# Kernel optimization log

Hardware: AMD Instinct MI355X
Metric: run time of the kernel (lower is better)

Reference implementation:

```python
import jax, jax.numpy as jnp
import numpy as np

K = 3      # kernel size
PAD = 1    # padding


def _conv(x, w, b=None):
    y = jax.lax.conv_general_dilated(
        x, w, window_strides=(1, 1), padding=((PAD, PAD), (PAD, PAD)),
        dimension_numbers=('NCHW', 'OIHW', 'NCHW'))
    if b is not None:
        y = y + b[None, :, None, None]
    return y


def _deform_conv2d(x, offset, mask, weight):
    # torchvision deform_conv2d with offset_groups == C (one offset pair per
    # input channel per kernel tap), stride=1, dilation=1, zero padding.
    B, C, H, W = x.shape
    KK = K * K
    off = offset.reshape(B, C, KK, 2, H, W)   # [...,0]=dy, [...,1]=dx
    dy, dx = off[:, :, :, 0], off[:, :, :, 1]
    m = mask.reshape(B, C, KK, H, W)

    ki = (jnp.arange(KK) // K).reshape(1, 1, KK, 1, 1).astype(x.dtype)
    kj = (jnp.arange(KK) % K).reshape(1, 1, KK, 1, 1).astype(x.dtype)
    gy = jnp.arange(H, dtype=x.dtype).reshape(1, 1, 1, H, 1)
    gx = jnp.arange(W, dtype=x.dtype).reshape(1, 1, 1, 1, W)
    py = dy + gy - PAD + ki   # sampling y coords, [B,C,KK,H,W]
    px = dx + gx - PAD + kj   # sampling x coords

    # torchvision: sample is zero unless -1 < p < size
    valid = (py > -1) & (py < H) & (px > -1) & (px < W)
    y0f = jnp.floor(py)
    x0f = jnp.floor(px)
    wy = py - y0f
    wx = px - x0f
    y0 = y0f.astype(jnp.int32)
    x0 = x0f.astype(jnp.int32)
    y1 = y0 + 1
    x1 = x0 + 1

    xf = x.reshape(B, C, H * W)

    def gather(yi, xi):
        inb = (yi >= 0) & (yi < H) & (xi >= 0) & (xi < W)
        yc = jnp.clip(yi, 0, H - 1)
        xc = jnp.clip(xi, 0, W - 1)
        idx = (yc * W + xc).reshape(B, C, -1)
        v = jnp.take_along_axis(xf, idx, axis=2).reshape(yi.shape)
        return jnp.where(inb, v, jnp.zeros((), x.dtype))

    val = ((1 - wy) * (1 - wx) * gather(y0, x0)
           + (1 - wy) * wx * gather(y0, x1)
           + wy * (1 - wx) * gather(y1, x0)
           + wy * wx * gather(y1, x1))
    samp = jnp.where(valid, val, jnp.zeros((), x.dtype)) * m   # [B,C,KK,H,W]

    O = weight.shape[0]
    return jnp.einsum('bckhw,ock->bohw', samp, weight.reshape(O, C, KK))


def setup_inputs() -> dict:
    key = jax.random.key(0)
    k1, k2, k3, k4, k5, k6 = jax.random.split(key, 6)
    B, C, O, H, W = 8, 64, 128, 64, 64
    KK = K * K
    x = jax.random.normal(k1, (B, C, H, W), dtype=jnp.float32)
    # offset conv: 2*C*KK output channels (module inits to 0; use small random
    # weights so the irregular sampling path is exercised)
    w_off = jax.random.normal(k2, (2 * C * KK, C, K, K), dtype=jnp.float32) * 0.05
    b_off = jnp.zeros((2 * C * KK,), dtype=jnp.float32)
    w_mod = jax.random.normal(k3, (C * KK, C, K, K), dtype=jnp.float32) * 0.05
    b_mod = jax.random.normal(k4, (C * KK,), dtype=jnp.float32) * 0.05
    w_conv = jax.random.normal(k5, (O, C, K, K), dtype=jnp.float32) / np.sqrt(C * KK)
    return {"x": x, "w_off": w_off, "b_off": b_off,
            "w_mod": w_mod, "b_mod": b_mod, "w_conv": w_conv}


def reference(x, w_off, b_off, w_mod, b_mod, w_conv):
    H, W = x.shape[2], x.shape[3]
    max_off = max(H, W) / 4.0
    offset = jnp.clip(_conv(x, w_off, b_off), -max_off, max_off)
    mask = _conv(x, w_mod, b_mod)
    return _deform_conv2d(x, offset, mask, w_conv)
```

## Files before the change

### kernel.cpp

```cpp
#include <hip/hip_runtime.h>
#include <cstddef>
#include <cstdint>

#define TCNT 256

namespace {
constexpr int CIN    = 64;
constexpr int COUT   = 128;
constexpr int HDIM   = 64;
constexpr int WDIM   = 64;
constexpr int HW     = HDIM * WDIM;
constexpr int KD     = CIN * 9;
constexpr int NOFF   = 2 * CIN * 9;
constexpr int NTOT   = NOFF + CIN * 9;
constexpr int NBATCH = 8;
constexpr int HXW    = 66;
constexpr int COPAD  = 1792;
constexpr int NGT    = COPAD / 16;
constexpr float MAXOFF = 16.0f;

constexpr size_t XT_ELEMS = (size_t)NBATCH * HXW * HXW * 64;
constexpr size_t WP_ELEMS = (size_t)18 * NGT * 512;
constexpr size_t WC_ELEMS = (size_t)18 * 8 * 512;
constexpr size_t OFF_XFH  = 0;
constexpr size_t OFF_WPH  = XT_ELEMS;
constexpr size_t OFF_WPL  = XT_ELEMS + WP_ELEMS;
constexpr size_t OFF_WCH  = XT_ELEMS + 2 * WP_ELEMS;
constexpr size_t FIXED_BYTES = (XT_ELEMS + 2 * WP_ELEMS + WC_ELEMS) * 2;
}

typedef __attribute__((ext_vector_type(8))) short    s16x8;
typedef __attribute__((ext_vector_type(8))) _Float16 f16x8;
typedef __attribute__((ext_vector_type(4))) float    f32x4;

__device__ __forceinline__ unsigned short f2h(float v) {
  _Float16 h = (_Float16)v;
  return __builtin_bit_cast(unsigned short, h);
}
__device__ __forceinline__ float h2f(unsigned short u) {
  return (float)__builtin_bit_cast(_Float16, u);
}

__global__ __launch_bounds__(TCNT) void prep_x(
    const float* __restrict__ x, unsigned short* __restrict__ xFh)
{
  const int b  = blockIdx.y;
  const int yy = blockIdx.x;
  const int t  = threadIdx.x;
  unsigned short* oh = xFh + ((size_t)(b * HXW + yy)) * HXW * 64;
  if (yy == 0 || yy == HXW - 1) {
    for (int lin = t; lin < HXW * 64; lin += TCNT) oh[lin] = 0;
    return;
  }
  __shared__ float tile[64][65];
  const int y = yy - 1;
  #pragma unroll
  for (int i = 0; i < 4; ++i) {
    const int f = t + TCNT * i;
    const int c = f >> 4, xq = f & 15;
    const float4 v =
        *(const float4*)(x + ((size_t)(b * 64 + c)) * HW + y * WDIM + xq * 4);
    tile[c][xq * 4 + 0] = v.x; tile[c][xq * 4 + 1] = v.y;
    tile[c][xq * 4 + 2] = v.z; tile[c][xq * 4 + 3] = v.w;
  }
  if (t < 128) {
    const int c = t & 63, xe = (t >> 6) ? (HXW - 1) * 64 : 0;
    oh[xe + c] = 0;
  }
  __syncthreads();
  const int xc = t >> 2, cg = (t & 3) * 16;
  s16x8 h0, h1;
  #pragma unroll
  for (int u = 0; u < 8; ++u) h0[u] = (short)f2h(tile[cg + u][xc]);
  #pragma unroll
  for (int u = 0; u < 8; ++u) h1[u] = (short)f2h(tile[cg + 8 + u][xc]);
  *(s16x8*)(oh + (xc + 1) * 64 + cg)     = h0;
  *(s16x8*)(oh + (xc + 1) * 64 + cg + 8) = h1;
}

__global__ __launch_bounds__(TCNT) void prep_w(
    const float* __restrict__ w_off, const float* __restrict__ w_mod,
    unsigned short* __restrict__ wF1h, unsigned short* __restrict__ wF1l)
{
  const int g  = blockIdx.x;
  const int hh = blockIdx.y;
  const int r  = hh >> 1, ks = hh & 1;
  const int t  = threadIdx.x;
  const size_t base = ((size_t)hh * NGT + g) * 512;
  #pragma unroll
  for (int q = 0; q < 2; ++q) {
    const int e = t + q * 256;
    const int l = e >> 3, f = e & 7;
    const int co = g * 16 + (l & 15);
    const int c  = ks * 32 + (l >> 4) * 8 + f;
    float v = 0.f;
    if (co < NOFF)      v = w_off[(size_t)co * KD + c * 9 + r];
    else if (co < NTOT) v = w_mod[(size_t)(co - NOFF) * KD + c * 9 + r];
    const unsigned short hb = f2h(v);
    wF1h[base + e] = hb;
    wF1l[base + e] = f2h(v - h2f(hb));
  }
}

__global__ __launch_bounds__(TCNT) void prep_wc(
    const float* __restrict__ w_conv, unsigned short* __restrict__ wF2)
{
  const int nt = blockIdx.x;
  const int hh = blockIdx.y;
  const int sc = hh >> 1, ks = hh & 1;
  const int t  = threadIdx.x;
  const size_t base = ((size_t)hh * 8 + nt) * 512;
  #pragma unroll
  for (int q = 0; q < 2; ++q) {
    const int e = t + q * 256;
    const int l = e >> 3, f = e & 7;
    const int o = nt * 16 + (l & 15);
    const int c = sc * 64 + ks * 32 + (l >> 4) * 8 + f;
    wF2[base + e] = f2h(w_conv[(size_t)o * KD + c]);
  }
}

__global__ __launch_bounds__(TCNT, 3) void dcn_stage1(
    const unsigned short* __restrict__ xFh,
    const unsigned short* __restrict__ wF1h, const unsigned short* __restrict__ wF1l,
    const float* __restrict__ b_off, const float* __restrict__ b_mod,
    float* __restrict__ ws, int b0, int nb)
{
  __shared__ unsigned short Ah[2][128][32];

  const int t      = threadIdx.x;
  const int Mchunk = nb * HW;
  const int p0  = blockIdx.x * 128;
  const int b   = b0 + (p0 >> 12);
  const int h0  = (p0 & (HW - 1)) >> 6;
  const int co0 = blockIdx.y * 128;

  const int s_row = t >> 1;
  const int s_kh  = t & 1;
  const int s_sw  = ((s_row >> 1) & 3) << 3;
  const int a_h   = h0 + (s_row >> 6);
  const int a_w   = s_row & 63;
  const unsigned short* xbh = xFh + (size_t)b * HXW * HXW * 64;

  const int wave = t >> 6, lane = t & 63;
  const int wm = wave >> 1, wn = wave & 1;
  const int lrow = lane & 15;
  const int lkh  = lane >> 4;
  const int gbase = (co0 >> 4) + wn * 4;

  f32x4 acc[4][4];
  #pragma unroll
  for (int m = 0; m < 4; ++m)
    #pragma unroll
    for (int n = 0; n < 4; ++n) acc[m][n] = (f32x4)0.f;

  s16x8 rE0, rE1, rO0, rO1;
  f16x8 wh[4], wl[4];

#define ALOAD(D0, D1, H)                                                     \
  {                                                                          \
    const int r_  = (H) >> 1;                                                \
    const int ks_ = (H) & 1;                                                 \
    const int ki_ = r_ / 3;                                                  \
    const int kj_ = r_ - 3 * ki_;                                            \
    const size_t aoff_ = ((size_t)((a_h + ki_) * HXW + (a_w + kj_))) * 64 +  \
                         ks_ * 32 + s_kh * 16;                               \
    D0 = *(const s16x8*)(xbh + aoff_);                                       \
    D1 = *(const s16x8*)(xbh + aoff_ + 8);                                   \
  }

#define AWRITE(S0, S1, SEL)                                                  \
  {                                                                          \
    const int c0_ = (s_kh * 16) ^ s_sw;                                      \
    const int c1_ = (s_kh * 16 + 8) ^ s_sw;                                  \
    *(s16x8*)&Ah[SEL][s_row][c0_] = S0;                                      \
    *(s16x8*)&Ah[SEL][s_row][c1_] = S1;                                      \
  }

#define WLOAD(H)                                                             \
  {                                                                          \
    _Pragma("unroll")                                                        \
    for (int n = 0; n < 4; ++n) {                                            \
      const size_t o_ = ((size_t)(H) * NGT + gbase + n) * 512 + lane * 8;    \
      wh[n] = *(const f16x8*)(wF1h + o_);                                    \
      wl[n] = *(const f16x8*)(wF1l + o_);                                    \
    }                                                                        \
  }

#define MFMA_P(SEL)                                                          \
  {                                                                          \
    f16x8 fa[4];                                                             \
    _Pragma("unroll")                                                        \
    for (int m = 0; m < 4; ++m) {                                            \
      const int row = wm * 64 + m * 16 + lrow;                               \
      const int col = (lkh * 8) ^ (((row >> 1) & 3) << 3);                   \
      fa[m] = *(const f16x8*)&Ah[SEL][row][col];                             \
    }                                                                        \
    _Pragma("unroll")                                                        \
    for (int n = 0; n < 4; ++n) {                                            \
      _Pragma("unroll")                                                      \
      for (int m = 0; m < 4; ++m) {                                          \
        acc[m][n] = __builtin_amdgcn_mfma_f32_16x16x32_f16(fa[m], wh[n], acc[m][n], 0, 0, 0); \
        acc[m][n] = __builtin_amdgcn_mfma_f32_16x16x32_f16(fa[m], wl[n], acc[m][n], 0, 0, 0); \
      }                                                                      \
    }                                                                        \
  }

  ALOAD(rE0, rE1, 0)
  WLOAD(0)
  AWRITE(rE0, rE1, 0)
  ALOAD(rO0, rO1, 1)
  __syncthreads();

  #pragma unroll 1
  for (int h = 0; h < 17; ++h) {
    MFMA_P(h & 1)
    WLOAD(h + 1)
    if ((h & 1) == 0) {
      AWRITE(rO0, rO1, 1)
      if (h < 16) ALOAD(rE0, rE1, h + 2)
    } else {
      AWRITE(rE0, rE1, 0)
      if (h < 16) ALOAD(rO0, rO1, h + 2)
    }
    __syncthreads();
  }
  MFMA_P(1)

  const bool isOff = (co0 < NOFF);
  #pragma unroll
  for (int n = 0; n < 4; ++n) {
    const int cog = co0 + wn * 64 + n * 16 + lrow;
    if (cog >= NTOT) continue;
    const float bias = isOff ? b_off[cog] : b_mod[cog - NOFF];
    float* oplane = ws + (size_t)cog * Mchunk;
    #pragma unroll
    for (int m = 0; m < 4; ++m) {
      f32x4 v = acc[m][n];
      float4 o;
      o.x = v[0] + bias; o.y = v[1] + bias; o.z = v[2] + bias; o.w = v[3] + bias;
      if (isOff) {
        o.x = fminf(MAXOFF, fmaxf(-MAXOFF, o.x));
        o.y = fminf(MAXOFF, fmaxf(-MAXOFF, o.y));
        o.z = fminf(MAXOFF, fmaxf(-MAXOFF, o.z));
        o.w = fminf(MAXOFF, fmaxf(-MAXOFF, o.w));
      }
      const int pb = p0 + wm * 64 + m * 16 + lkh * 4;
      *(float4*)(oplane + pb) = o;
    }
  }
#undef ALOAD
#undef AWRITE
#undef WLOAD
#undef MFMA_P
}

__global__ __launch_bounds__(TCNT) void dcn_stage2(
    const float* __restrict__ x, const float* __restrict__ planes,
    const unsigned short* __restrict__ wF2,
    float* __restrict__ out, int b0, int nb)
{
  __shared__ unsigned short SH[2][32][64], SL[2][32][64];

  const int t      = threadIdx.x;
  const int Mchunk = nb * HW;
  const int pc0 = blockIdx.x * 32;
  const int b   = b0 + (pc0 >> 12);
  const int h   = (pc0 & (HW - 1)) >> 6;
  const int w0  = pc0 & 63;

  const int tpx = t & 31;
  const int tsg = t >> 5;
  const int a_swz = (tpx & 7) << 3;
  const float* ws_pix = planes + pc0 + tpx;
  const float* xb     = x + (size_t)b * CIN * HW;

  const int wave = t >> 6, lane = t & 63;
  const int lrow = lane & 15, lkh = lane >> 4;
  const int f_swz = (lrow & 7) << 3;

  f32x4 acc[2][2];
  #pragma unroll
  for (int m = 0; m < 2; ++m)
    #pragma unroll
    for (int n = 0; n < 2; ++n) acc[m][n] = (f32x4)0.f;

  float vals[8];
  f16x8 w4A[4], w4B[4];

#define SAMPLE(SCC)                                                          \
  {                                                                          \
    _Pragma("unroll")                                                        \
    for (int j = 0; j < 8; ++j) {                                            \
      const int sl = tsg * 8 + j;                                            \
      const int s  = (SCC) * 64 + sl;                                        \
      const int c  = s / 9;                                                  \
      const int kk = s - c * 9;                                              \
      const int ki = kk / 3;                                                 \
      const int kj = kk - ki * 3;                                            \
      const float dy = ws_pix[(size_t)(2 * s)     * Mchunk];                 \
      const float dx = ws_pix[(size_t)(2 * s + 1) * Mchunk];                 \
      const float m  = ws_pix[(size_t)(NOFF + s)  * Mchunk];                 \
      const float py = dy + (float)(h + ki - 1);                             \
      const float px = dx + (float)(w0 + tpx + kj - 1);                      \
      const bool valid = (py > -1.f) && (py < (float)HDIM) &&                \
                         (px > -1.f) && (px < (float)WDIM);                  \
      const float y0f = floorf(py), x0f = floorf(px);                        \
      const float wy = py - y0f, wx = px - x0f;                              \
      const int y0 = (int)y0f, x0 = (int)x0f;                                \
      const float* plane = xb + c * HW;                                      \
      float v00 = 0.f, v01 = 0.f, v10 = 0.f, v11 = 0.f;                      \
      if ((unsigned)y0 < (unsigned)HDIM) {                                   \
        const float* row = plane + (y0 << 6);                                \
        if ((unsigned)x0       < (unsigned)WDIM) v00 = row[x0];              \
        if ((unsigned)(x0 + 1) < (unsigned)WDIM) v01 = row[x0 + 1];          \
      }                                                                      \
      if ((unsigned)(y0 + 1) < (unsigned)HDIM) {                             \
        const float* row = plane + ((y0 + 1) << 6);                          \
        if ((unsigned)x0       < (unsigned)WDIM) v10 = row[x0];              \
        if ((unsigned)(x0 + 1) < (unsigned)WDIM) v11 = row[x0 + 1];          \
      }                                                                      \
      const float val = (1.f - wy) * ((1.f - wx) * v00 + wx * v01)           \
                      + wy         * ((1.f - wx) * v10 + wx * v11);          \
      vals[j] = valid ? val * m : 0.f;                                       \
    }                                                                        \
  }

#define PACK(SEL)                                                            \
  {                                                                          \
    s16x8 h8, l8;                                                            \
    _Pragma("unroll")                                                        \
    for (int u = 0; u < 8; ++u) {                                            \
      const unsigned short hb = f2h(vals[u]);                                \
      h8[u] = (short)hb;                                                     \
      l8[u] = (short)f2h(vals[u] - h2f(hb));                                 \
    }                                                                        \
    const int col = (tsg * 8) ^ a_swz;                                       \
    *(s16x8*)&SH[SEL][tpx][col] = h8;                                        \
    *(s16x8*)&SL[SEL][tpx][col] = l8;                                        \
  }

#define W2LOAD(DST, SCC)                                                     \
  {                                                                          \
    _Pragma("unroll")                                                        \
    for (int ks = 0; ks < 2; ++ks)                                           \
      _Pragma("unroll")                                                      \
      for (int n = 0; n < 2; ++n) {                                          \
        const size_t o_ = (((size_t)(SCC) * 2 + ks) * 8 + wave * 2 + n) * 512\
                          + lane * 8;                                        \
        DST[ks * 2 + n] = *(const f16x8*)(wF2 + o_);                         \
      }                                                                      \
  }

#define MFMA2(SEL, WREG)                                                     \
  {                                                                          \
    _Pragma("unroll")                                                        \
    for (int ks = 0; ks < 2; ++ks) {                                         \
      const int colb = (ks * 32 + lkh * 8) ^ f_swz;                          \
      f16x8 fah[2], fal[2];                                                  \
      _Pragma("unroll")                                                      \
      for (int m = 0; m < 2; ++m) {                                          \
        fah[m] = *(const f16x8*)&SH[SEL][m * 16 + lrow][colb];               \
        fal[m] = *(const f16x8*)&SL[SEL][m * 16 + lrow][colb];               \
      }                                                                      \
      _Pragma("unroll")                                                      \
      for (int n = 0; n < 2; ++n) {                                          \
        _Pragma("unroll")                                                    \
        for (int m = 0; m < 2; ++m) {                                        \
          acc[m][n] = __builtin_amdgcn_mfma_f32_16x16x32_f16(fah[m], WREG[ks * 2 + n], acc[m][n], 0, 0, 0); \
          acc[m][n] = __builtin_amdgcn_mfma_f32_16x16x32_f16(fal[m], WREG[ks * 2 + n], acc[m][n], 0, 0, 0); \
        }                                                                    \
      }                                                                      \
    }                                                                        \
  }

  SAMPLE(0)
  PACK(0)
  W2LOAD(w4A, 0)
  __syncthreads();

  #pragma unroll 1
  for (int it = 0; it < 4; ++it) {
    const int sce = 2 * it;
    W2LOAD(w4B, sce + 1)
    SAMPLE(sce + 1)
    MFMA2(0, w4A)
    PACK(1)
    __syncthreads();
    W2LOAD(w4A, sce + 2)
    SAMPLE(sce + 2)
    MFMA2(1, w4B)
    PACK(0)
    __syncthreads();
  }
  MFMA2(0, w4A)

  #pragma unroll
  for (int n = 0; n < 2; ++n) {
    const int o = wave * 32 + n * 16 + lrow;
    float* obase = out + ((size_t)(b * COUT + o)) * HW + h * WDIM + w0;
    #pragma unroll
    for (int m = 0; m < 2; ++m) {
      const int pxl = m * 16 + lkh * 4;
      f32x4 v = acc[m][n];
      *(float4*)(obase + pxl) = make_float4(v[0], v[1], v[2], v[3]);
    }
  }
#undef SAMPLE
#undef PACK
#undef W2LOAD
#undef MFMA2
}

extern "C" void kernel_launch(void* const* d_in, const int* in_sizes, int n_in,
                              void* d_out, int out_size, void* d_ws, size_t ws_size,
                              hipStream_t stream) {
  (void)in_sizes; (void)n_in; (void)out_size;
  const float* x      = (const float*)d_in[0];
  const float* w_off  = (const float*)d_in[1];
  const float* b_off  = (const float*)d_in[2];
  const float* w_mod  = (const float*)d_in[3];
  const float* b_mod  = (const float*)d_in[4];
  const float* w_conv = (const float*)d_in[5];
  float* out = (float*)d_out;

  unsigned short* wsu = (unsigned short*)d_ws;
  unsigned short* xFh  = wsu + OFF_XFH;
  unsigned short* wF1h = wsu + OFF_WPH;
  unsigned short* wF1l = wsu + OFF_WPL;
  unsigned short* wF2  = wsu + OFF_WCH;
  float* planes = (float*)((char*)d_ws + FIXED_BYTES);

  const size_t ws_per_batch = (size_t)NTOT * HW * sizeof(float);
  size_t avail = (ws_size > FIXED_BYTES) ? (ws_size - FIXED_BYTES) : 0;
  int nb = (int)(avail / ws_per_batch);
  if (nb < 1) nb = 1;
  if (nb > NBATCH) nb = NBATCH;

  prep_x<<<dim3(HXW, NBATCH), TCNT, 0, stream>>>(x, xFh);
  prep_w<<<dim3(NGT, 18), TCNT, 0, stream>>>(w_off, w_mod, wF1h, wF1l);
  prep_wc<<<dim3(8, 18), TCNT, 0, stream>>>(w_conv, wF2);

  for (int b0 = 0; b0 < NBATCH; b0 += nb) {
    const int cur = (NBATCH - b0 < nb) ? (NBATCH - b0) : nb;
    dim3 g1(cur * 32, 14);
    dcn_stage1<<<g1, TCNT, 0, stream>>>(xFh, wF1h, wF1l, b_off, b_mod,
                                        planes, b0, cur);
    dcn_stage2<<<cur * 128, TCNT, 0, stream>>>(x, planes, wF2, out, b0, cur);
  }
}
```

Baseline: 303.1 us.

## Sample from padded fp16 channel-last x and drop split-fp16 low part in stage2

Stage2 now gathers bilinear samples from the zero-padded fp16 NHWC copy of x instead of the fp32 NCHW input. Clamping the corner coordinates into the pad border removes the per-corner bounds branches. The sampled values are packed as a single fp16 instead of a hi/lo pair, which halves the MFMA count and LDS traffic in stage2. It also swaps __syncthreads for a barrier that only waits on LDS counters, so outstanding global loads are not drained. The cost is lower precision, because x and the sampled values are now rounded to fp16.

```diff
diff --git a/kernel.cpp b/kernel.cpp
--- a/kernel.cpp
+++ b/kernel.cpp
@@ -41,6 +41,9 @@
   return (float)__builtin_bit_cast(_Float16, u);
 }
 
+#define BARR() { asm volatile("s_waitcnt lgkmcnt(0)" ::: "memory");          \
+                 __builtin_amdgcn_s_barrier(); }
+
 __global__ __launch_bounds__(TCNT) void prep_x(
     const float* __restrict__ x, unsigned short* __restrict__ xFh)
 {
@@ -210,7 +213,7 @@
   WLOAD(0)
   AWRITE(rE0, rE1, 0)
   ALOAD(rO0, rO1, 1)
-  __syncthreads();
+  BARR()
 
   #pragma unroll 1
   for (int h = 0; h < 17; ++h) {
@@ -223,7 +226,7 @@
       AWRITE(rE0, rE1, 0)
       if (h < 16) ALOAD(rO0, rO1, h + 2)
     }
-    __syncthreads();
+    BARR()
   }
   MFMA_P(1)
 
@@ -256,11 +259,11 @@
 }
 
 __global__ __launch_bounds__(TCNT) void dcn_stage2(
-    const float* __restrict__ x, const float* __restrict__ planes,
+    const unsigned short* __restrict__ xFh, const float* __restrict__ planes,
     const unsigned short* __restrict__ wF2,
     float* __restrict__ out, int b0, int nb)
 {
-  __shared__ unsigned short SH[2][32][64], SL[2][32][64];
+  __shared__ unsigned short SH[2][32][64];
 
   const int t      = threadIdx.x;
   const int Mchunk = nb * HW;
@@ -273,7 +276,7 @@
   const int tsg = t >> 5;
   const int a_swz = (tpx & 7) << 3;
   const float* ws_pix = planes + pc0 + tpx;
-  const float* xb     = x + (size_t)b * CIN * HW;
+  const unsigned short* xbF = xFh + (size_t)b * HXW * HXW * 64;
 
   const int wave = t >> 6, lane = t & 63;
   const int lrow = lane & 15, lkh = lane >> 4;
@@ -307,19 +310,14 @@
                          (px > -1.f) && (px < (float)WDIM);                  \
       const float y0f = floorf(py), x0f = floorf(px);                        \
       const float wy = py - y0f, wx = px - x0f;                              \
-      const int y0 = (int)y0f, x0 = (int)x0f;                                \
-      const float* plane = xb + c * HW;                                      \
-      float v00 = 0.f, v01 = 0.f, v10 = 0.f, v11 = 0.f;                      \
-      if ((unsigned)y0 < (unsigned)HDIM) {                                   \
-        const float* row = plane + (y0 << 6);                                \
-        if ((unsigned)x0       < (unsigned)WDIM) v00 = row[x0];              \
-        if ((unsigned)(x0 + 1) < (unsigned)WDIM) v01 = row[x0 + 1];          \
-      }                                                                      \
-      if ((unsigned)(y0 + 1) < (unsigned)HDIM) {                             \
-        const float* row = plane + ((y0 + 1) << 6);                          \
-        if ((unsigned)x0       < (unsigned)WDIM) v10 = row[x0];              \
-        if ((unsigned)(x0 + 1) < (unsigned)WDIM) v11 = row[x0 + 1];          \
-      }                                                                      \
+      int y0 = (int)y0f, x0 = (int)x0f;                                      \
+      y0 = min(max(y0, -1), 63);              \
+      x0 = min(max(x0, -1), 63);              \
+      const int addr = ((y0 + 1) * HXW + (x0 + 1)) * 64 + c;                 \
+      const float v00 = h2f(xbF[addr]);                                      \
+      const float v01 = h2f(xbF[addr + 64]);                                 \
+      const float v10 = h2f(xbF[addr + HXW * 64]);                           \
+      const float v11 = h2f(xbF[addr + HXW * 64 + 64]);                      \
       const float val = (1.f - wy) * ((1.f - wx) * v00 + wx * v01)           \
                       + wy         * ((1.f - wx) * v10 + wx * v11);          \
       vals[j] = valid ? val * m : 0.f;                                       \
@@ -328,16 +326,11 @@
 
 #define PACK(SEL)                                                            \
   {                                                                          \
-    s16x8 h8, l8;                                                            \
-    _Pragma("unroll")                                                        \
-    for (int u = 0; u < 8; ++u) {                                            \
-      const unsigned short hb = f2h(vals[u]);                                \
-      h8[u] = (short)hb;                                                     \
-      l8[u] = (short)f2h(vals[u] - h2f(hb));                                 \
-    }                                                                        \
+    s16x8 h8;                                                                \
+    _Pragma("unroll")                                                        \
+    for (int u = 0; u < 8; ++u) h8[u] = (short)f2h(vals[u]);                 \
     const int col = (tsg * 8) ^ a_swz;                                       \
     *(s16x8*)&SH[SEL][tpx][col] = h8;                                        \
-    *(s16x8*)&SL[SEL][tpx][col] = l8;                                        \
   }
 
 #define W2LOAD(DST, SCC)                                                     \
@@ -357,27 +350,22 @@
     _Pragma("unroll")                                                        \
     for (int ks = 0; ks < 2; ++ks) {                                         \
       const int colb = (ks * 32 + lkh * 8) ^ f_swz;                          \
-      f16x8 fah[2], fal[2];                                                  \
+      f16x8 fah[2];                                                          \
       _Pragma("unroll")                                                      \
-      for (int m = 0; m < 2; ++m) {                                          \
+      for (int m = 0; m < 2; ++m)                                            \
         fah[m] = *(const f16x8*)&SH[SEL][m * 16 + lrow][colb];               \
-        fal[m] = *(const f16x8*)&SL[SEL][m * 16 + lrow][colb];               \
-      }                                                                      \
       _Pragma("unroll")                                                      \
-      for (int n = 0; n < 2; ++n) {                                          \
+      for (int n = 0; n < 2; ++n)                                            \
         _Pragma("unroll")                                                    \
-        for (int m = 0; m < 2; ++m) {                                        \
+        for (int m = 0; m < 2; ++m)                                          \
           acc[m][n] = __builtin_amdgcn_mfma_f32_16x16x32_f16(fah[m], WREG[ks * 2 + n], acc[m][n], 0, 0, 0); \
-          acc[m][n] = __builtin_amdgcn_mfma_f32_16x16x32_f16(fal[m], WREG[ks * 2 + n], acc[m][n], 0, 0, 0); \
-        }                                                                    \
-      }                                                                      \
     }                                                                        \
   }
 
   SAMPLE(0)
   PACK(0)
   W2LOAD(w4A, 0)
-  __syncthreads();
+  BARR()
 
   #pragma unroll 1
   for (int it = 0; it < 4; ++it) {
@@ -386,12 +374,12 @@
     SAMPLE(sce + 1)
     MFMA2(0, w4A)
     PACK(1)
-    __syncthreads();
+    BARR()
     W2LOAD(w4A, sce + 2)
     SAMPLE(sce + 2)
     MFMA2(1, w4B)
     PACK(0)
-    __syncthreads();
+    BARR()
   }
   MFMA2(0, w4A)
 
@@ -446,6 +434,6 @@
     dim3 g1(cur * 32, 14);
     dcn_stage1<<<g1, TCNT, 0, stream>>>(xFh, wF1h, wF1l, b_off, b_mod,
                                         planes, b0, cur);
-    dcn_stage2<<<cur * 128, TCNT, 0, stream>>>(x, planes, wF2, out, b0, cur);
-  }
-}
+    dcn_stage2<<<cur * 128, TCNT, 0, stream>>>(xFh, planes, wF2, out, b0, cur);
+  }
+}
```

Measured after the change: 409.4 us. 35.1% more time.
